# Kernel optimization log

Hardware: AMD Instinct MI355X
Metric: run time of the kernel (lower is better)

## Reference

```python
import jax, jax.numpy as jnp
import numpy as np

N_NODES = 50000


def _gcn_layer(x, src, dst, deg_inv_sqrt, W, b):
    # GCNConv (PyG defaults): h = x @ W; out = D^-1/2 (A+I) D^-1/2 h + b
    h = x @ W
    norm = deg_inv_sqrt[src] * deg_inv_sqrt[dst]          # [E]
    msg = h[src] * norm[:, None]                           # [E, d_out]
    agg = jax.ops.segment_sum(msg, dst, num_segments=N_NODES)
    agg = agg + h * (deg_inv_sqrt * deg_inv_sqrt)[:, None]  # self-loop term
    return agg + b


def _stack(x, src, dst, dis, W1, b1, W2, b2, W3, b3):
    h = jax.nn.relu(_gcn_layer(x, src, dst, dis, W1, b1))
    h = jax.nn.relu(_gcn_layer(h, src, dst, dis, W2, b2))
    return jax.nn.relu(_gcn_layer(h, src, dst, dis, W3, b3))


def setup_inputs() -> dict:
    key = jax.random.key(0)
    ks = jax.random.split(key, 16)
    din, lat, E = 128, 64, 800000
    x = jax.random.normal(ks[0], (N_NODES, din), dtype=jnp.float32)
    edge_index = jax.random.randint(ks[1], (2, E), 0, N_NODES, dtype=jnp.int64)

    def lin(k, fan_in, fan_out):
        s = 1.0 / np.sqrt(fan_in)
        kw, kb = jax.random.split(k)
        W = jax.random.uniform(kw, (fan_in, fan_out), minval=-s, maxval=s, dtype=jnp.float32)
        b = jax.random.uniform(kb, (fan_out,), minval=-s, maxval=s, dtype=jnp.float32)
        return W, b

    Wm1, bm1 = lin(ks[2], din, 64)
    Wm2, bm2 = lin(ks[3], 64, 128)
    Wm3, bm3 = lin(ks[4], 128, lat)
    Wl1, bl1 = lin(ks[5], din, 64)
    Wl2, bl2 = lin(ks[6], 64, 128)
    Wl3, bl3 = lin(ks[7], 128, lat)
    return {"x": x, "edge_index": edge_index,
            "Wm1": Wm1, "bm1": bm1, "Wm2": Wm2, "bm2": bm2, "Wm3": Wm3, "bm3": bm3,
            "Wl1": Wl1, "bl1": bl1, "Wl2": Wl2, "bl2": bl2, "Wl3": Wl3, "bl3": bl3}


def reference(x, edge_index, Wm1, bm1, Wm2, bm2, Wm3, bm3, Wl1, bl1, Wl2, bl2, Wl3, bl3):
    src, dst = edge_index[0], edge_index[1]
    # degree with self-loops (PyG: deg over dst of A+I)
    deg = jax.ops.segment_sum(jnp.ones_like(dst, dtype=x.dtype), dst, num_segments=N_NODES) + 1.0
    dis = jax.lax.rsqrt(deg)
    mu = _stack(x, src, dst, dis, Wm1, bm1, Wm2, bm2, Wm3, bm3)
    log = _stack(x, src, dst, dis, Wl1, bl1, Wl2, bl2, Wl3, bl3)
    return (mu, log)
```

## Files before the change

### kernel.cpp

```cpp
#include <hip/hip_runtime.h>

#define N_NODES_C 50000

__global__ void detect_kernel(const int* __restrict__ w, int ncheck, int* __restrict__ flag) {
    int tid = blockIdx.x * blockDim.x + threadIdx.x;
    if (tid < ncheck) {
        if (w[2 * tid + 1] != 0) *flag = 0;
    }
}

__global__ void count_kernel(const int* __restrict__ ei, int E, const int* __restrict__ flag,
                             int* __restrict__ counts) {
    int e = blockIdx.x * blockDim.x + threadIdx.x;
    if (e >= E) return;
    int shift = (*flag != 0) ? 1 : 0;
    int d = ei[(unsigned)(E + e) << shift];
    atomicAdd(&counts[d], 1);
}

__global__ void dis_kernel(const int* __restrict__ counts, float* __restrict__ dis, int n) {
    int i = blockIdx.x * blockDim.x + threadIdx.x;
    if (i < n) dis[i] = rsqrtf((float)counts[i] + 1.0f);
}

__global__ void scan_kernel(const int* __restrict__ counts, int* __restrict__ row_start,
                            int* __restrict__ cursor, int n) {
    __shared__ int wsum[16];
    __shared__ int carry;
    __shared__ int chunk_total;
    int tid = threadIdx.x;
    int lane = tid & 63;
    int wid = tid >> 6;
    if (tid == 0) carry = 0;
    __syncthreads();
    for (int base = 0; base < n; base += 1024) {
        int i = base + tid;
        int v = (i < n) ? counts[i] : 0;
        int x = v;
        #pragma unroll
        for (int off = 1; off < 64; off <<= 1) {
            int y = __shfl_up(x, off);
            if (lane >= off) x += y;
        }
        if (lane == 63) wsum[wid] = x;
        __syncthreads();
        if (tid == 0) {
            int run = 0;
            #pragma unroll
            for (int q = 0; q < 16; q++) { int t = wsum[q]; wsum[q] = run; run += t; }
            chunk_total = run;
        }
        __syncthreads();
        int excl = x - v + wsum[wid] + carry;
        if (i < n) { row_start[i] = excl; cursor[i] = excl; }
        __syncthreads();
        if (tid == 0) carry += chunk_total;
        __syncthreads();
    }
    if (tid == 0) row_start[n] = carry;
}

__global__ void fill_kernel(const int* __restrict__ ei, int E, const int* __restrict__ flag,
                            const float* __restrict__ dis, int* __restrict__ cursor,
                            int* __restrict__ csr_src, float* __restrict__ csr_w) {
    int e = blockIdx.x * blockDim.x + threadIdx.x;
    if (e >= E) return;
    int shift = (*flag != 0) ? 1 : 0;
    int s = ei[(unsigned)e << shift];
    int d = ei[(unsigned)(E + e) << shift];
    int pos = atomicAdd(&cursor[d], 1);
    csr_src[pos] = s;
    csr_w[pos] = dis[s] * dis[d];
}

template <bool FINAL>
__global__ __launch_bounds__(256) void agg128_kernel(const float* __restrict__ h,
                                                     const int* __restrict__ row_start,
                                                     const int* __restrict__ csr_src,
                                                     const float* __restrict__ csr_w,
                                                     const float* __restrict__ dis,
                                                     const float* __restrict__ bmu,
                                                     const float* __restrict__ blog,
                                                     float* __restrict__ out,
                                                     float* __restrict__ outlog, int M) {
    int wid = threadIdx.x >> 6;
    int lane = threadIdx.x & 63;
    int node = blockIdx.x * 4 + wid;
    if (node >= M) return;
    int half = lane >> 5;
    int c0 = (lane & 31) * 4;

    int s = row_start[node];
    int e = row_start[node + 1];

    float a0 = 0.f, a1 = 0.f, a2 = 0.f, a3 = 0.f;
    int i = s + half;
    for (; i + 2 < e; i += 4) {
        int s0 = csr_src[i];
        int s1 = csr_src[i + 2];
        float w0 = csr_w[i];
        float w1 = csr_w[i + 2];
        float4 v0 = *(const float4*)&h[(size_t)s0 * 128 + c0];
        float4 v1 = *(const float4*)&h[(size_t)s1 * 128 + c0];
        a0 = fmaf(w0, v0.x, a0); a1 = fmaf(w0, v0.y, a1);
        a2 = fmaf(w0, v0.z, a2); a3 = fmaf(w0, v0.w, a3);
        a0 = fmaf(w1, v1.x, a0); a1 = fmaf(w1, v1.y, a1);
        a2 = fmaf(w1, v1.z, a2); a3 = fmaf(w1, v1.w, a3);
    }
    if (i < e) {
        int s0 = csr_src[i];
        float w0 = csr_w[i];
        float4 v0 = *(const float4*)&h[(size_t)s0 * 128 + c0];
        a0 = fmaf(w0, v0.x, a0); a1 = fmaf(w0, v0.y, a1);
        a2 = fmaf(w0, v0.z, a2); a3 = fmaf(w0, v0.w, a3);
    }
    a0 += __shfl_xor(a0, 32);
    a1 += __shfl_xor(a1, 32);
    a2 += __shfl_xor(a2, 32);
    a3 += __shfl_xor(a3, 32);

    float dn = dis[node];
    float sw = dn * dn;
    float4 sv = *(const float4*)&h[(size_t)node * 128 + c0];
    a0 = fmaf(sw, sv.x, a0); a1 = fmaf(sw, sv.y, a1);
    a2 = fmaf(sw, sv.z, a2); a3 = fmaf(sw, sv.w, a3);

    if (half == 0) {
        if constexpr (FINAL) {
            float b0, b1, b2, b3;
            float* yp;
            if (c0 < 64) {
                b0 = bmu[c0]; b1 = bmu[c0 + 1]; b2 = bmu[c0 + 2]; b3 = bmu[c0 + 3];
                yp = out + (size_t)node * 64 + c0;
            } else {
                int c = c0 - 64;
                b0 = blog[c]; b1 = blog[c + 1]; b2 = blog[c + 2]; b3 = blog[c + 3];
                yp = outlog + (size_t)node * 64 + c;
            }
            float4 o;
            o.x = fmaxf(a0 + b0, 0.f);
            o.y = fmaxf(a1 + b1, 0.f);
            o.z = fmaxf(a2 + b2, 0.f);
            o.w = fmaxf(a3 + b3, 0.f);
            *(float4*)yp = o;
        } else {
            *(float4*)&out[(size_t)node * 128 + c0] = make_float4(a0, a1, a2, a3);
        }
    }
}

template <int K, int N, int LDXS, int XA, int XB, int BM, int KCH, bool RELU>
__global__ __launch_bounds__(256) void gemm2_kernel(const float* __restrict__ X,
                                                    const float* __restrict__ Wa,
                                                    const float* __restrict__ Wb,
                                                    const float* __restrict__ ba,
                                                    const float* __restrict__ bb,
                                                    float* __restrict__ Y, int ldy, int M) {
    constexpr int NTX = N / 8;
    constexpr int NTY = 256 / NTX;
    constexpr int RPT = BM / NTY;
    constexpr int XLD = LDXS + 4;
    constexpr int NH = N / 2;
    __shared__ alignas(16) float xs[BM * XLD];
    __shared__ alignas(16) float ws[KCH * N];

    int t = threadIdx.x;
    int row0 = blockIdx.x * BM;

    constexpr int KQ = LDXS / 4;
    for (int i = t; i < BM * KQ; i += 256) {
        int r = i / KQ, kq = i % KQ;
        float4 v = make_float4(0.f, 0.f, 0.f, 0.f);
        if (row0 + r < M) v = *(const float4*)&X[(size_t)(row0 + r) * LDXS + 4 * kq];
        *(float4*)&xs[r * XLD + 4 * kq] = v;
    }

    int tx = t % NTX;
    int ty = t / NTX;
    float acc[RPT][8];
    #pragma unroll
    for (int rr = 0; rr < RPT; rr++)
        #pragma unroll
        for (int j = 0; j < 8; j++) acc[rr][j] = 0.f;

    for (int kc = 0; kc < K; kc += KCH) {
        __syncthreads();
        constexpr int NQ = N / 4;
        constexpr int HQ = NH / 4;
        for (int i = t; i < KCH * NQ; i += 256) {
            int kk = i / NQ, cq = i % NQ;
            float4 v;
            if (cq < HQ) v = *(const float4*)&Wa[(size_t)(kc + kk) * NH + 4 * cq];
            else         v = *(const float4*)&Wb[(size_t)(kc + kk) * NH + 4 * (cq - HQ)];
            *(float4*)&ws[kk * N + 4 * cq] = v;
        }
        __syncthreads();

        #pragma unroll 4
        for (int kk = 0; kk < KCH; ++kk) {
            int k = kc + kk;
            float4 wa = *(const float4*)&ws[kk * N + tx * 4];
            float4 wb = *(const float4*)&ws[kk * N + NH + tx * 4];
            #pragma unroll
            for (int rr = 0; rr < RPT; rr++) {
                int rbase = (ty * RPT + rr) * XLD;
                float xa = xs[rbase + XA + k];
                acc[rr][0] = fmaf(xa, wa.x, acc[rr][0]);
                acc[rr][1] = fmaf(xa, wa.y, acc[rr][1]);
                acc[rr][2] = fmaf(xa, wa.z, acc[rr][2]);
                acc[rr][3] = fmaf(xa, wa.w, acc[rr][3]);
                float xb;
                if constexpr (XA == XB) xb = xa;
                else xb = xs[rbase + XB + k];
                acc[rr][4] = fmaf(xb, wb.x, acc[rr][4]);
                acc[rr][5] = fmaf(xb, wb.y, acc[rr][5]);
                acc[rr][6] = fmaf(xb, wb.z, acc[rr][6]);
                acc[rr][7] = fmaf(xb, wb.w, acc[rr][7]);
            }
        }
    }

    int ca = tx * 4;
    float4 bva = *(const float4*)&ba[ca];
    float4 bvb = *(const float4*)&bb[ca];
    #pragma unroll
    for (int rr = 0; rr < RPT; rr++) {
        int row = row0 + ty * RPT + rr;
        if (row < M) {
            float4 oa, ob;
            oa.x = acc[rr][0] + bva.x; oa.y = acc[rr][1] + bva.y;
            oa.z = acc[rr][2] + bva.z; oa.w = acc[rr][3] + bva.w;
            ob.x = acc[rr][4] + bvb.x; ob.y = acc[rr][5] + bvb.y;
            ob.z = acc[rr][6] + bvb.z; ob.w = acc[rr][7] + bvb.w;
            if constexpr (RELU) {
                oa.x = fmaxf(oa.x, 0.f); oa.y = fmaxf(oa.y, 0.f);
                oa.z = fmaxf(oa.z, 0.f); oa.w = fmaxf(oa.w, 0.f);
                ob.x = fmaxf(ob.x, 0.f); ob.y = fmaxf(ob.y, 0.f);
                ob.z = fmaxf(ob.z, 0.f); ob.w = fmaxf(ob.w, 0.f);
            }
            *(float4*)&Y[(size_t)row * ldy + ca] = oa;
            *(float4*)&Y[(size_t)row * ldy + NH + ca] = ob;
        }
    }
}

extern "C" void kernel_launch(void* const* d_in, const int* in_sizes, int n_in,
                              void* d_out, int out_size, void* d_ws, size_t ws_size,
                              hipStream_t stream) {
    const float* x   = (const float*)d_in[0];
    const int*   ei  = (const int*)d_in[1];
    const float* Wm1 = (const float*)d_in[2];  const float* bm1 = (const float*)d_in[3];
    const float* Wm2 = (const float*)d_in[4];  const float* bm2 = (const float*)d_in[5];
    const float* Wm3 = (const float*)d_in[6];  const float* bm3 = (const float*)d_in[7];
    const float* Wl1 = (const float*)d_in[8];  const float* bl1 = (const float*)d_in[9];
    const float* Wl2 = (const float*)d_in[10]; const float* bl2 = (const float*)d_in[11];
    const float* Wl3 = (const float*)d_in[12]; const float* bl3 = (const float*)d_in[13];
    float* out = (float*)d_out;

    const int M = N_NODES_C;
    const int E = in_sizes[1] / 2;

    char* ws = (char*)d_ws;
    size_t off = 0;
    auto alloc = [&](size_t bytes) {
        size_t o = off;
        off += (bytes + 255) & ~(size_t)255;
        return o;
    };
    int*   flag      = (int*)(ws + alloc(4));
    int*   counts    = (int*)(ws + alloc((size_t)M * 4));
    int*   row_start = (int*)(ws + alloc((size_t)(M + 1) * 4));
    int*   cursor    = (int*)(ws + alloc((size_t)M * 4));
    float* dis       = (float*)(ws + alloc((size_t)M * 4));
    int*   csr_src   = (int*)(ws + alloc((size_t)E * 4));
    float* csr_w     = (float*)(ws + alloc((size_t)E * 4));
    float* bufA      = (float*)(ws + alloc((size_t)M * 256 * 4));
    float* bufB      = (float*)(ws + alloc((size_t)M * 256 * 4));

    hipMemsetAsync(flag, 1, 4, stream);
    hipMemsetAsync(counts, 0, (size_t)M * 4, stream);

    int ncheck = (E < 2048) ? E : 2048;
    detect_kernel<<<(ncheck + 255) / 256, 256, 0, stream>>>(ei, ncheck, flag);
    count_kernel<<<(E + 255) / 256, 256, 0, stream>>>(ei, E, flag, counts);
    dis_kernel<<<(M + 255) / 256, 256, 0, stream>>>(counts, dis, M);
    scan_kernel<<<1, 1024, 0, stream>>>(counts, row_start, cursor, M);
    fill_kernel<<<(E + 255) / 256, 256, 0, stream>>>(ei, E, flag, dis, cursor, csr_src, csr_w);

    int ablocks = (M + 3) / 4;

    agg128_kernel<false><<<ablocks, 256, 0, stream>>>(x, row_start, csr_src, csr_w, dis,
                                                      nullptr, nullptr, bufA, nullptr, M);

    gemm2_kernel<128, 128, 128, 0, 0, 64, 32, true><<<(M + 63) / 64, 256, 0, stream>>>(
        bufA, Wm1, Wl1, bm1, bl1, bufB, 128, M);

    agg128_kernel<false><<<ablocks, 256, 0, stream>>>(bufB, row_start, csr_src, csr_w, dis,
                                                      nullptr, nullptr, bufA, nullptr, M);

    gemm2_kernel<64, 256, 128, 0, 64, 32, 32, true><<<(M + 31) / 32, 256, 0, stream>>>(
        bufA, Wm2, Wl2, bm2, bl2, bufB, 256, M);

    float* zb = (float*)(ws + alloc(64 * 4));
    hipMemsetAsync(zb, 0, 64 * 4, stream);
    gemm2_kernel<128, 128, 256, 0, 128, 32, 32, false><<<(M + 31) / 32, 256, 0, stream>>>(
        bufB, Wm3, Wl3, zb, zb, bufA, 128, M);

    agg128_kernel<true><<<ablocks, 256, 0, stream>>>(bufA, row_start, csr_src, csr_w, dis,
                                                     bm3, bl3, out, out + (size_t)M * 64, M);
}
```

Baseline: 520.2 us.

## Drop stored edge weights, unroll gather, and rework GEMM with transposed weight tiles

Edge weights are no longer stored in CSR. The aggregation kernel computes them on the fly from dis[src]*dis[node] and unrolls the neighbour gather to four edges per half-wave. The dis computation moves into the scan kernel, which removes one launch and one pass. The GEMM now keeps weights transposed in shared memory, reads float4 along K for both X and W, and takes new tile and thread counts plus a no-bias variant that replaces the memset of a zero buffer. The cost is an extra random gather of dis per edge, and the scattered strided output stores may coalesce less well.

```diff
diff --git a/kernel.cpp b/kernel.cpp
--- a/kernel.cpp
+++ b/kernel.cpp
@@ -18,13 +18,8 @@
     atomicAdd(&counts[d], 1);
 }
 
-__global__ void dis_kernel(const int* __restrict__ counts, float* __restrict__ dis, int n) {
-    int i = blockIdx.x * blockDim.x + threadIdx.x;
-    if (i < n) dis[i] = rsqrtf((float)counts[i] + 1.0f);
-}
-
 __global__ void scan_kernel(const int* __restrict__ counts, int* __restrict__ row_start,
-                            int* __restrict__ cursor, int n) {
+                            int* __restrict__ cursor, float* __restrict__ dis, int n) {
     __shared__ int wsum[16];
     __shared__ int carry;
     __shared__ int chunk_total;
@@ -52,7 +47,11 @@
         }
         __syncthreads();
         int excl = x - v + wsum[wid] + carry;
-        if (i < n) { row_start[i] = excl; cursor[i] = excl; }
+        if (i < n) {
+            row_start[i] = excl;
+            cursor[i] = excl;
+            dis[i] = rsqrtf((float)v + 1.0f);
+        }
         __syncthreads();
         if (tid == 0) carry += chunk_total;
         __syncthreads();
@@ -61,8 +60,7 @@
 }
 
 __global__ void fill_kernel(const int* __restrict__ ei, int E, const int* __restrict__ flag,
-                            const float* __restrict__ dis, int* __restrict__ cursor,
-                            int* __restrict__ csr_src, float* __restrict__ csr_w) {
+                            int* __restrict__ cursor, int* __restrict__ csr_src) {
     int e = blockIdx.x * blockDim.x + threadIdx.x;
     if (e >= E) return;
     int shift = (*flag != 0) ? 1 : 0;
@@ -70,14 +68,12 @@
     int d = ei[(unsigned)(E + e) << shift];
     int pos = atomicAdd(&cursor[d], 1);
     csr_src[pos] = s;
-    csr_w[pos] = dis[s] * dis[d];
 }
 
 template <bool FINAL>
 __global__ __launch_bounds__(256) void agg128_kernel(const float* __restrict__ h,
                                                      const int* __restrict__ row_start,
                                                      const int* __restrict__ csr_src,
-                                                     const float* __restrict__ csr_w,
                                                      const float* __restrict__ dis,
                                                      const float* __restrict__ bmu,
                                                      const float* __restrict__ blog,
@@ -92,24 +88,35 @@
 
     int s = row_start[node];
     int e = row_start[node + 1];
+    float dn = dis[node];
 
     float a0 = 0.f, a1 = 0.f, a2 = 0.f, a3 = 0.f;
     int i = s + half;
-    for (; i + 2 < e; i += 4) {
+    for (; i + 6 < e; i += 8) {
         int s0 = csr_src[i];
         int s1 = csr_src[i + 2];
-        float w0 = csr_w[i];
-        float w1 = csr_w[i + 2];
+        int s2 = csr_src[i + 4];
+        int s3 = csr_src[i + 6];
+        float w0 = dis[s0] * dn;
+        float w1 = dis[s1] * dn;
+        float w2 = dis[s2] * dn;
+        float w3 = dis[s3] * dn;
         float4 v0 = *(const float4*)&h[(size_t)s0 * 128 + c0];
         float4 v1 = *(const float4*)&h[(size_t)s1 * 128 + c0];
+        float4 v2 = *(const float4*)&h[(size_t)s2 * 128 + c0];
+        float4 v3 = *(const float4*)&h[(size_t)s3 * 128 + c0];
         a0 = fmaf(w0, v0.x, a0); a1 = fmaf(w0, v0.y, a1);
         a2 = fmaf(w0, v0.z, a2); a3 = fmaf(w0, v0.w, a3);
         a0 = fmaf(w1, v1.x, a0); a1 = fmaf(w1, v1.y, a1);
         a2 = fmaf(w1, v1.z, a2); a3 = fmaf(w1, v1.w, a3);
-    }
-    if (i < e) {
+        a0 = fmaf(w2, v2.x, a0); a1 = fmaf(w2, v2.y, a1);
+        a2 = fmaf(w2, v2.z, a2); a3 = fmaf(w2, v2.w, a3);
+        a0 = fmaf(w3, v3.x, a0); a1 = fmaf(w3, v3.y, a1);
+        a2 = fmaf(w3, v3.z, a2); a3 = fmaf(w3, v3.w, a3);
+    }
+    for (; i < e; i += 2) {
         int s0 = csr_src[i];
-        float w0 = csr_w[i];
+        float w0 = dis[s0] * dn;
         float4 v0 = *(const float4*)&h[(size_t)s0 * 128 + c0];
         a0 = fmaf(w0, v0.x, a0); a1 = fmaf(w0, v0.y, a1);
         a2 = fmaf(w0, v0.z, a2); a3 = fmaf(w0, v0.w, a3);
@@ -119,7 +126,6 @@
     a2 += __shfl_xor(a2, 32);
     a3 += __shfl_xor(a3, 32);
 
-    float dn = dis[node];
     float sw = dn * dn;
     float4 sv = *(const float4*)&h[(size_t)node * 128 + c0];
     a0 = fmaf(sw, sv.x, a0); a1 = fmaf(sw, sv.y, a1);
@@ -149,26 +155,29 @@
     }
 }
 
-template <int K, int N, int LDXS, int XA, int XB, int BM, int KCH, bool RELU>
-__global__ __launch_bounds__(256) void gemm2_kernel(const float* __restrict__ X,
-                                                    const float* __restrict__ Wa,
-                                                    const float* __restrict__ Wb,
-                                                    const float* __restrict__ ba,
-                                                    const float* __restrict__ bb,
-                                                    float* __restrict__ Y, int ldy, int M) {
+template <int K, int N, int LDXS, int XA, int XB, int BM, int KCH, int NT,
+          bool RELU, bool BIAS>
+__global__ __launch_bounds__(NT) void gemm3_kernel(const float* __restrict__ X,
+                                                   const float* __restrict__ Wa,
+                                                   const float* __restrict__ Wb,
+                                                   const float* __restrict__ ba,
+                                                   const float* __restrict__ bb,
+                                                   float* __restrict__ Y, int ldy, int M) {
     constexpr int NTX = N / 8;
-    constexpr int NTY = 256 / NTX;
+    constexpr int NTY = NT / NTX;
     constexpr int RPT = BM / NTY;
     constexpr int XLD = LDXS + 4;
     constexpr int NH = N / 2;
+    constexpr int WTS = KCH + 4;
+    constexpr int TPB = NTX / 2;
     __shared__ alignas(16) float xs[BM * XLD];
-    __shared__ alignas(16) float ws[KCH * N];
+    __shared__ alignas(16) float wst[N * WTS];
 
     int t = threadIdx.x;
     int row0 = blockIdx.x * BM;
 
     constexpr int KQ = LDXS / 4;
-    for (int i = t; i < BM * KQ; i += 256) {
+    for (int i = t; i < BM * KQ; i += NT) {
         int r = i / KQ, kq = i % KQ;
         float4 v = make_float4(0.f, 0.f, 0.f, 0.f);
         if (row0 + r < M) v = *(const float4*)&X[(size_t)(row0 + r) * LDXS + 4 * kq];
@@ -177,6 +186,11 @@
 
     int tx = t % NTX;
     int ty = t / NTX;
+    int branch = (tx >= TPB) ? 1 : 0;
+    int txl = tx - branch * TPB;
+    int xoff = branch ? XB : XA;
+    int wbase = (branch * NH + txl) * WTS;
+
     float acc[RPT][8];
     #pragma unroll
     for (int rr = 0; rr < RPT; rr++)
@@ -185,61 +199,55 @@
 
     for (int kc = 0; kc < K; kc += KCH) {
         __syncthreads();
-        constexpr int NQ = N / 4;
-        constexpr int HQ = NH / 4;
-        for (int i = t; i < KCH * NQ; i += 256) {
-            int kk = i / NQ, cq = i % NQ;
-            float4 v;
-            if (cq < HQ) v = *(const float4*)&Wa[(size_t)(kc + kk) * NH + 4 * cq];
-            else         v = *(const float4*)&Wb[(size_t)(kc + kk) * NH + 4 * (cq - HQ)];
-            *(float4*)&ws[kk * N + 4 * cq] = v;
-        }
-        __syncthreads();
-
-        #pragma unroll 4
-        for (int kk = 0; kk < KCH; ++kk) {
-            int k = kc + kk;
-            float4 wa = *(const float4*)&ws[kk * N + tx * 4];
-            float4 wb = *(const float4*)&ws[kk * N + NH + tx * 4];
+        for (int i = t; i < KCH * N; i += NT) {
+            int kk = i / N, c = i % N;
+            float v = (c < NH) ? Wa[(size_t)(kc + kk) * NH + c]
+                               : Wb[(size_t)(kc + kk) * NH + (c - NH)];
+            wst[c * WTS + kk] = v;
+        }
+        __syncthreads();
+
+        #pragma unroll
+        for (int kk4 = 0; kk4 < KCH / 4; ++kk4) {
+            float4 wv[8];
+            #pragma unroll
+            for (int j = 0; j < 8; j++)
+                wv[j] = *(const float4*)&wst[wbase + j * (TPB * WTS) + 4 * kk4];
             #pragma unroll
             for (int rr = 0; rr < RPT; rr++) {
-                int rbase = (ty * RPT + rr) * XLD;
-                float xa = xs[rbase + XA + k];
-                acc[rr][0] = fmaf(xa, wa.x, acc[rr][0]);
-                acc[rr][1] = fmaf(xa, wa.y, acc[rr][1]);
-                acc[rr][2] = fmaf(xa, wa.z, acc[rr][2]);
-                acc[rr][3] = fmaf(xa, wa.w, acc[rr][3]);
-                float xb;
-                if constexpr (XA == XB) xb = xa;
-                else xb = xs[rbase + XB + k];
-                acc[rr][4] = fmaf(xb, wb.x, acc[rr][4]);
-                acc[rr][5] = fmaf(xb, wb.y, acc[rr][5]);
-                acc[rr][6] = fmaf(xb, wb.z, acc[rr][6]);
-                acc[rr][7] = fmaf(xb, wb.w, acc[rr][7]);
+                float4 xv = *(const float4*)&xs[(ty * RPT + rr) * XLD + xoff + kc + 4 * kk4];
+                #pragma unroll
+                for (int j = 0; j < 8; j++) {
+                    acc[rr][j] = fmaf(xv.x, wv[j].x, acc[rr][j]);
+                    acc[rr][j] = fmaf(xv.y, wv[j].y, acc[rr][j]);
+                    acc[rr][j] = fmaf(xv.z, wv[j].z, acc[rr][j]);
+                    acc[rr][j] = fmaf(xv.w, wv[j].w, acc[rr][j]);
+                }
             }
         }
     }
 
-    int ca = tx * 4;
-    float4 bva = *(const float4*)&ba[ca];
-    float4 bvb = *(const float4*)&bb[ca];
+    float bj[8];
+    #pragma unroll
+    for (int j = 0; j < 8; j++) {
+        if constexpr (BIAS) {
+            const float* bp = branch ? bb : ba;
+            bj[j] = bp[txl + j * TPB];
+        } else {
+            bj[j] = 0.f;
+        }
+    }
     #pragma unroll
     for (int rr = 0; rr < RPT; rr++) {
         int row = row0 + ty * RPT + rr;
         if (row < M) {
-            float4 oa, ob;
-            oa.x = acc[rr][0] + bva.x; oa.y = acc[rr][1] + bva.y;
-            oa.z = acc[rr][2] + bva.z; oa.w = acc[rr][3] + bva.w;
-            ob.x = acc[rr][4] + bvb.x; ob.y = acc[rr][5] + bvb.y;
-            ob.z = acc[rr][6] + bvb.z; ob.w = acc[rr][7] + bvb.w;
-            if constexpr (RELU) {
-                oa.x = fmaxf(oa.x, 0.f); oa.y = fmaxf(oa.y, 0.f);
-                oa.z = fmaxf(oa.z, 0.f); oa.w = fmaxf(oa.w, 0.f);
-                ob.x = fmaxf(ob.x, 0.f); ob.y = fmaxf(ob.y, 0.f);
-                ob.z = fmaxf(ob.z, 0.f); ob.w = fmaxf(ob.w, 0.f);
+            float* yp = Y + (size_t)row * ldy + branch * NH + txl;
+            #pragma unroll
+            for (int j = 0; j < 8; j++) {
+                float o = acc[rr][j] + bj[j];
+                if constexpr (RELU) o = fmaxf(o, 0.f);
+                yp[j * TPB] = o;
             }
-            *(float4*)&Y[(size_t)row * ldy + ca] = oa;
-            *(float4*)&Y[(size_t)row * ldy + NH + ca] = ob;
         }
     }
 }
@@ -273,7 +281,6 @@
     int*   cursor    = (int*)(ws + alloc((size_t)M * 4));
     float* dis       = (float*)(ws + alloc((size_t)M * 4));
     int*   csr_src   = (int*)(ws + alloc((size_t)E * 4));
-    float* csr_w     = (float*)(ws + alloc((size_t)E * 4));
     float* bufA      = (float*)(ws + alloc((size_t)M * 256 * 4));
     float* bufB      = (float*)(ws + alloc((size_t)M * 256 * 4));
 
@@ -283,29 +290,26 @@
     int ncheck = (E < 2048) ? E : 2048;
     detect_kernel<<<(ncheck + 255) / 256, 256, 0, stream>>>(ei, ncheck, flag);
     count_kernel<<<(E + 255) / 256, 256, 0, stream>>>(ei, E, flag, counts);
-    dis_kernel<<<(M + 255) / 256, 256, 0, stream>>>(counts, dis, M);
-    scan_kernel<<<1, 1024, 0, stream>>>(counts, row_start, cursor, M);
-    fill_kernel<<<(E + 255) / 256, 256, 0, stream>>>(ei, E, flag, dis, cursor, csr_src, csr_w);
+    scan_kernel<<<1, 1024, 0, stream>>>(counts, row_start, cursor, dis, M);
+    fill_kernel<<<(E + 255) / 256, 256, 0, stream>>>(ei, E, flag, cursor, csr_src);
 
     int ablocks = (M + 3) / 4;
 
-    agg128_kernel<false><<<ablocks, 256, 0, stream>>>(x, row_start, csr_src, csr_w, dis,
+    agg128_kernel<false><<<ablocks, 256, 0, stream>>>(x, row_start, csr_src, dis,
                                                       nullptr, nullptr, bufA, nullptr, M);
 
-    gemm2_kernel<128, 128, 128, 0, 0, 64, 32, true><<<(M + 63) / 64, 256, 0, stream>>>(
-        bufA, Wm1, Wl1, bm1, bl1, bufB, 128, M);
-
-    agg128_kernel<false><<<ablocks, 256, 0, stream>>>(bufB, row_start, csr_src, csr_w, dis,
+    gemm3_kernel<128, 128, 128, 0, 0, 64, 32, 256, true, true>
+        <<<(M + 63) / 64, 256, 0, stream>>>(bufA, Wm1, Wl1, bm1, bl1, bufB, 128, M);
+
+    agg128_kernel<false><<<ablocks, 256, 0, stream>>>(bufB, row_start, csr_src, dis,
                                                       nullptr, nullptr, bufA, nullptr, M);
 
-    gemm2_kernel<64, 256, 128, 0, 64, 32, 32, true><<<(M + 31) / 32, 256, 0, stream>>>(
-        bufA, Wm2, Wl2, bm2, bl2, bufB, 256, M);
-
-    float* zb = (float*)(ws + alloc(64 * 4));
-    hipMemsetAsync(zb, 0, 64 * 4, stream);
-    gemm2_kernel<128, 128, 256, 0, 128, 32, 32, false><<<(M + 31) / 32, 256, 0, stream>>>(
-        bufB, Wm3, Wl3, zb, zb, bufA, 128, M);
-
-    agg128_kernel<true><<<ablocks, 256, 0, stream>>>(bufA, row_start, csr_src, csr_w, dis,
+    gemm3_kernel<64, 256, 128, 0, 64, 64, 16, 256, true, true>
+        <<<(M + 63) / 64, 256, 0, stream>>>(bufA, Wm2, Wl2, bm2, bl2, bufB, 256, M);
+
+    gemm3_kernel<128, 128, 256, 0, 128, 32, 32, 128, false, false>
+        <<<(M + 31) / 32, 128, 0, stream>>>(bufB, Wm3, Wl3, nullptr, nullptr, bufA, 128, M);
+
+    agg128_kernel<true><<<ablocks, 256, 0, stream>>>(bufA, row_start, csr_src, dis,
                                                      bm3, bl3, out, out + (size_t)M * 64, M);
 }
```

Result: slower. 569.7 us (+9.5%).
